# Kernel tuning notes

Measured on AMD Instinct MI355X. Metric: run time of the kernel, lower is better.

## Reference

```python
import jax, jax.numpy as jnp
import numpy as np

DIM = 1024
E = 8
K = 2
EPS = 1e-5

def _ln(x, g, b):
    mu = jnp.mean(x, axis=-1, keepdims=True)
    var = jnp.mean(jnp.square(x - mu), axis=-1, keepdims=True)
    return (x - mu) * jax.lax.rsqrt(var + EPS) * g + b

def setup_inputs() -> dict:
    key = jax.random.key(0)
    ks = jax.random.split(key, 8)
    H = 2 * DIM
    s_in = 1.0 / np.sqrt(DIM)
    s_h = 1.0 / np.sqrt(H)
    return {
        "x": jax.random.normal(ks[0], (2, 2048, DIM), dtype=jnp.float32),
        "gate_w": jax.random.uniform(ks[1], (DIM, E), minval=-s_in, maxval=s_in, dtype=jnp.float32),
        "w1": jax.random.uniform(ks[2], (E, DIM, H), minval=-s_in, maxval=s_in, dtype=jnp.float32),
        "b1": jax.random.uniform(ks[3], (E, H), minval=-s_in, maxval=s_in, dtype=jnp.float32),
        "ln1_g": jnp.ones((E, H), dtype=jnp.float32),
        "ln1_b": jnp.zeros((E, H), dtype=jnp.float32),
        "w2": jax.random.uniform(ks[4], (E, H, DIM), minval=-s_h, maxval=s_h, dtype=jnp.float32),
        "b2": jax.random.uniform(ks[5], (E, DIM), minval=-s_h, maxval=s_h, dtype=jnp.float32),
        "ln_g": jnp.ones((DIM,), dtype=jnp.float32),
        "ln_b": jnp.zeros((DIM,), dtype=jnp.float32),
    }

def reference(x, gate_w, w1, b1, ln1_g, ln1_b, w2, b2, ln_g, ln_b):
    shape = x.shape
    xf = x.reshape(-1, shape[-1])                      # [T, D]
    gates = jax.nn.softmax(xf @ gate_w, axis=-1)       # [T, E]
    topw, topi = jax.lax.top_k(gates, K)               # [T, K]
    topw = topw / jnp.sum(topw, axis=-1, keepdims=True)
    # combine weights per expert: [T, E]
    combine = jnp.sum(topw[:, :, None] * jax.nn.one_hot(topi, E, dtype=xf.dtype), axis=1)
    # run all experts on all tokens (vectorized grouped GEMM), combine by gate mask
    h = jnp.einsum('td,edh->teh', xf, w1) + b1          # [T, E, 2D]
    h = _ln(h, ln1_g, ln1_b)
    h = jax.nn.gelu(h, approximate=False)
    y = jnp.einsum('teh,ehd->ted', h, w2) + b2          # [T, E, D]
    out = jnp.einsum('ted,te->td', y, combine)          # [T, D]
    out = _ln(out + xf, ln_g, ln_b)
    return out.reshape(shape)
```

## Files before the change

### kernel.cpp

```cpp
#include <hip/hip_runtime.h>
#include <hip/hip_bf16.h>

#define DIMX 1024
#define HID  2048
#define NE   8
#define NT   4096
#define NPAIR 8192
#define MAXSTRIP 72

typedef __attribute__((ext_vector_type(8))) __bf16 bf16x8;
typedef __attribute__((ext_vector_type(4))) float f32x4;

__device__ inline unsigned short f2bf(float f) {
  union { float f; unsigned u; } v; v.f = f;
  unsigned r = v.u + 0x7FFFu + ((v.u >> 16) & 1u);
  return (unsigned short)(r >> 16);
}
__device__ inline float bf2f(unsigned short h) {
  union { unsigned u; float f; } v; v.u = ((unsigned)h) << 16;
  return v.f;
}

__device__ __forceinline__ void gload_lds16(const unsigned short* g, unsigned short* l) {
  __builtin_amdgcn_global_load_lds(
      (const __attribute__((address_space(1))) unsigned int*)g,
      (__attribute__((address_space(3))) unsigned int*)l, 16, 0, 0);
}

#define O_CNT   0u
#define O_TOK   1024u
#define O_TK    132096u
#define O_PW    263168u
#define O_TI    394240u
#define O_TW    427008u
#define O_POFF  459776u
#define O_SE    459904u
#define O_SR0   460416u
#define O_XBF   524288u
#define O_W1T   16777216u
#define O_W2T   50331648u
#define O_H     83886080u
#define O_Y     121634816u

__global__ __launch_bounds__(256) void k_gate_cvt(const float* __restrict__ x,
                                                  const float* __restrict__ gw,
                                                  unsigned short* __restrict__ xbf,
                                                  int* __restrict__ ti,
                                                  float* __restrict__ tw) {
  int t = blockIdx.x * 4 + (threadIdx.x >> 6);
  int lane = threadIdx.x & 63;
  const float4* xr = (const float4*)(x + (size_t)t * DIMX);
  ushort4* xo = (ushort4*)(xbf + (size_t)t * DIMX);
  float p[NE];
#pragma unroll
  for (int e = 0; e < NE; e++) p[e] = 0.f;
#pragma unroll
  for (int j = 0; j < 4; j++) {
    int idx4 = j * 64 + lane;
    float4 v = xr[idx4];
    ushort4 o; o.x = f2bf(v.x); o.y = f2bf(v.y); o.z = f2bf(v.z); o.w = f2bf(v.w);
    xo[idx4] = o;
    const float4* gp = (const float4*)(gw + (size_t)(idx4 * 4) * NE);
    float4 gA = gp[0], gB = gp[1], gC = gp[2], gD = gp[3];
    float4 gE = gp[4], gF = gp[5], gG = gp[6], gH = gp[7];
    p[0] += v.x * gA.x + v.y * gC.x + v.z * gE.x + v.w * gG.x;
    p[1] += v.x * gA.y + v.y * gC.y + v.z * gE.y + v.w * gG.y;
    p[2] += v.x * gA.z + v.y * gC.z + v.z * gE.z + v.w * gG.z;
    p[3] += v.x * gA.w + v.y * gC.w + v.z * gE.w + v.w * gG.w;
    p[4] += v.x * gB.x + v.y * gD.x + v.z * gF.x + v.w * gH.x;
    p[5] += v.x * gB.y + v.y * gD.y + v.z * gF.y + v.w * gH.y;
    p[6] += v.x * gB.z + v.y * gD.z + v.z * gF.z + v.w * gH.z;
    p[7] += v.x * gB.w + v.y * gD.w + v.z * gF.w + v.w * gH.w;
  }
#pragma unroll
  for (int e = 0; e < NE; e++)
#pragma unroll
    for (int off = 32; off > 0; off >>= 1) p[e] += __shfl_xor(p[e], off);
  if (lane == 0) {
    int ia = 0; float va = p[0];
#pragma unroll
    for (int e = 1; e < NE; e++) if (p[e] > va) { va = p[e]; ia = e; }
    int ib = -1; float vb = -3.0e38f;
#pragma unroll
    for (int e = 0; e < NE; e++) { if (e == ia) continue; if (p[e] > vb) { vb = p[e]; ib = e; } }
    float w0 = 1.f / (1.f + expf(vb - va));
    ti[t * 2] = ia;     tw[t * 2] = w0;
    ti[t * 2 + 1] = ib; tw[t * 2 + 1] = 1.f - w0;
  }
}

__global__ __launch_bounds__(512) void k_build(const int* __restrict__ ti,
                                               const float* __restrict__ tw,
                                               int* __restrict__ cnt,
                                               int* __restrict__ poffs,
                                               int* __restrict__ s_e, int* __restrict__ s_r0,
                                               int* __restrict__ ptok, int* __restrict__ ptk,
                                               float* __restrict__ pw) {
  __shared__ int sti[NPAIR];
  __shared__ float stw[NPAIR];
  __shared__ int scnt[NE];
  for (int i = threadIdx.x; i < NPAIR; i += 512) { sti[i] = ti[i]; stw[i] = tw[i]; }
  __syncthreads();
  int wid = threadIdx.x >> 6;
  int lane = threadIdx.x & 63;
  int c = 0;
  for (int p = lane; p < NPAIR; p += 64) c += (sti[p] == wid) ? 1 : 0;
#pragma unroll
  for (int off = 32; off > 0; off >>= 1) c += __shfl_xor(c, off);
  if (lane == 0) scnt[wid] = c;
  __syncthreads();
  if (threadIdx.x == 0) {
    int s = 0, pacc = 0;
    for (int e = 0; e < NE; e++) {
      cnt[e] = scnt[e];
      poffs[e] = pacc;
      int ns = (scnt[e] + 127) >> 7;
      for (int k = 0; k < ns; k++) { s_e[s] = e; s_r0[s] = k * 128; s++; }
      pacc += ns * 128;
    }
    poffs[NE] = pacc;
    for (; s < MAXSTRIP; s++) { s_e[s] = -1; s_r0[s] = 0; }
  }
  int base = 0;
  for (int p0 = 0; p0 < NPAIR; p0 += 64) {
    int p = p0 + lane;
    bool m = (sti[p] == wid);
    unsigned long long mask = __ballot(m);
    if (m) {
      int pos = base + __popcll(mask & ((1ull << lane) - 1ull));
      ptok[wid * NT + pos] = p >> 1;
      ptk[wid * NT + pos] = p;
      pw[wid * NT + pos] = stw[p];
    }
    base += __popcll(mask);
  }
}

__global__ __launch_bounds__(256) void k_transpose_cvt(const float* __restrict__ in,
                                                       unsigned short* __restrict__ out,
                                                       int R, int C) {
  __shared__ float tile[64][73];
  int e = blockIdx.z;
  const float* ip = in + (size_t)e * R * C;
  unsigned short* op = out + (size_t)e * R * C;
  int c0 = blockIdx.x * 64, r0 = blockIdx.y * 64;
  int tx = threadIdx.x & 15, ty = threadIdx.x >> 4;
#pragma unroll
  for (int i = 0; i < 4; i++) {
    int row = ty + i * 16;
    float4 v = *(const float4*)(ip + (size_t)(r0 + row) * C + c0 + tx * 4);
    tile[row][tx * 4] = v.x; tile[row][tx * 4 + 1] = v.y;
    tile[row][tx * 4 + 2] = v.z; tile[row][tx * 4 + 3] = v.w;
  }
  __syncthreads();
  int rx = threadIdx.x & 15, cy = threadIdx.x >> 4;
  int r_off = rx * 4;
#pragma unroll
  for (int i = 0; i < 4; i++) {
    int cc = cy + i * 16;
    ushort4 h;
    h.x = f2bf(tile[r_off][cc]);     h.y = f2bf(tile[r_off + 1][cc]);
    h.z = f2bf(tile[r_off + 2][cc]); h.w = f2bf(tile[r_off + 3][cc]);
    *(ushort4*)(op + (size_t)(c0 + cc) * R + r0 + r_off) = h;
  }
}

#define BM 128
#define BN 128
#define BK 32

__global__ __launch_bounds__(256) void k_gemm1(
    const unsigned short* __restrict__ xbf,
    const unsigned short* __restrict__ w1t,
    const float* __restrict__ bias1,
    const int* __restrict__ cnt, const int* __restrict__ s_e,
    const int* __restrict__ s_r0, const int* __restrict__ poffs,
    const int* __restrict__ ptok,
    unsigned short* __restrict__ hpre)
{
  int s = blockIdx.y;
  int e = s_e[s];
  if (e < 0) return;
  int r0e = s_r0[s];
  int n_e = cnt[e];
  int pbase = poffs[e];
  int col0 = blockIdx.x * BN;

  __shared__ __align__(16) unsigned short As[2][BM][BK];
  __shared__ __align__(16) unsigned short Bs[2][BN][BK];

  int tid = threadIdx.x;
  int lane = tid & 63, wid = tid >> 6;
  int wr = wid >> 1, wc = wid & 1;
  int quad = lane >> 4, m16 = lane & 15;

  int rr = lane >> 2;
  int csrc = ((lane & 3) ^ ((lane >> 3) & 3)) * 8;
  int ga0 = r0e + wid * 32 + rr;      if (ga0 >= n_e) ga0 = n_e - 1;
  int ga1 = r0e + wid * 32 + 16 + rr; if (ga1 >= n_e) ga1 = n_e - 1;
  int t0 = ptok[e * NT + ga0];
  int t1 = ptok[e * NT + ga1];
  const unsigned short* a0p = xbf + (size_t)t0 * DIMX + csrc;
  const unsigned short* a1p = xbf + (size_t)t1 * DIMX + csrc;
  const unsigned short* bbase = w1t + (size_t)e * HID * DIMX;
  const unsigned short* b0p = bbase + (size_t)(col0 + wid * 32 + rr) * DIMX + csrc;
  const unsigned short* b1p = bbase + (size_t)(col0 + wid * 32 + 16 + rr) * DIMX + csrc;

  int ca = (quad ^ ((m16 >> 1) & 3)) * 8;

  f32x4 acc[4][4];
#pragma unroll
  for (int i = 0; i < 4; i++)
#pragma unroll
    for (int j = 0; j < 4; j++) acc[i][j] = (f32x4)(0.f);

#define STAGE1(b, kk) do { \
    gload_lds16(a0p + (kk), &As[b][wid * 32][0]); \
    gload_lds16(a1p + (kk), &As[b][wid * 32 + 16][0]); \
    gload_lds16(b0p + (kk), &Bs[b][wid * 32][0]); \
    gload_lds16(b1p + (kk), &Bs[b][wid * 32 + 16][0]); \
  } while (0)

  STAGE1(0, 0);
  __syncthreads();
  int cur = 0;
  for (int k0 = 0; k0 < DIMX; k0 += BK) {
    if (k0 + BK < DIMX) STAGE1(cur ^ 1, k0 + BK);
    bf16x8 af[4], bfr[4];
#pragma unroll
    for (int i = 0; i < 4; i++) af[i]  = *(const bf16x8*)&As[cur][wr * 64 + i * 16 + m16][ca];
#pragma unroll
    for (int j = 0; j < 4; j++) bfr[j] = *(const bf16x8*)&Bs[cur][wc * 64 + j * 16 + m16][ca];
#pragma unroll
    for (int i = 0; i < 4; i++)
#pragma unroll
      for (int j = 0; j < 4; j++)
        acc[i][j] = __builtin_amdgcn_mfma_f32_16x16x32_bf16(af[i], bfr[j], acc[i][j], 0, 0, 0);
    __syncthreads();
    cur ^= 1;
  }
#undef STAGE1

  float bj[4];
#pragma unroll
  for (int j = 0; j < 4; j++) bj[j] = bias1[e * HID + col0 + wc * 64 + j * 16 + m16];
#pragma unroll
  for (int i = 0; i < 4; i++) {
#pragma unroll
    for (int r = 0; r < 4; r++) {
      int g = r0e + wr * 64 + i * 16 + quad * 4 + r;
      if (g < n_e) {
        size_t rowbase = (size_t)(pbase + g) * HID;
#pragma unroll
        for (int j = 0; j < 4; j++) {
          int colg = col0 + wc * 64 + j * 16 + m16;
          hpre[rowbase + colg] = f2bf(acc[i][j][r] + bj[j]);
        }
      }
    }
  }
}

__global__ __launch_bounds__(256) void k_ln_gelu(unsigned short* __restrict__ h,
                                                 const float* __restrict__ g1,
                                                 const float* __restrict__ bb1,
                                                 const int* __restrict__ s_e) {
  int row = blockIdx.x * 4 + (threadIdx.x >> 6);
  int e = s_e[row >> 7];
  if (e < 0) return;
  int lane = threadIdx.x & 63;
  unsigned short* p = h + (size_t)row * HID;
  int4* p4 = (int4*)p;
  int4 raw[4];
#pragma unroll
  for (int sg = 0; sg < 4; sg++) raw[sg] = p4[sg * 64 + lane];
  float v[32];
#pragma unroll
  for (int sg = 0; sg < 4; sg++) {
    const unsigned short* u = (const unsigned short*)&raw[sg];
#pragma unroll
    for (int k = 0; k < 8; k++) v[sg * 8 + k] = bf2f(u[k]);
  }
  float s = 0.f;
#pragma unroll
  for (int i = 0; i < 32; i++) s += v[i];
#pragma unroll
  for (int off = 32; off > 0; off >>= 1) s += __shfl_xor(s, off);
  float mean = s * (1.f / HID);
  float sq = 0.f;
#pragma unroll
  for (int i = 0; i < 32; i++) { float d = v[i] - mean; sq += d * d; }
#pragma unroll
  for (int off = 32; off > 0; off >>= 1) sq += __shfl_xor(sq, off);
  float rstd = rsqrtf(sq * (1.f / HID) + 1e-5f);
  const float4* gg = (const float4*)(g1 + (size_t)e * HID);
  const float4* gb = (const float4*)(bb1 + (size_t)e * HID);
#pragma unroll
  for (int sg = 0; sg < 4; sg++) {
    float4 ga = gg[sg * 128 + lane * 2], gc = gg[sg * 128 + lane * 2 + 1];
    float4 ba = gb[sg * 128 + lane * 2], bc = gb[sg * 128 + lane * 2 + 1];
    float gn[8] = {ga.x, ga.y, ga.z, ga.w, gc.x, gc.y, gc.z, gc.w};
    float bn[8] = {ba.x, ba.y, ba.z, ba.w, bc.x, bc.y, bc.z, bc.w};
    unsigned short o[8];
#pragma unroll
    for (int k = 0; k < 8; k++) {
      float xn = (v[sg * 8 + k] - mean) * rstd * gn[k] + bn[k];
      float ge = 0.5f * xn * (1.f + erff(xn * 0.7071067811865476f));
      o[k] = f2bf(ge);
    }
    p4[sg * 64 + lane] = *(const int4*)o;
  }
}

__global__ __launch_bounds__(256) void k_gemm2(
    const unsigned short* __restrict__ hb,
    const unsigned short* __restrict__ w2t,
    const float* __restrict__ bias2,
    const int* __restrict__ cnt, const int* __restrict__ s_e,
    const int* __restrict__ s_r0, const int* __restrict__ poffs,
    const int* __restrict__ ptk, const float* __restrict__ pw,
    float* __restrict__ ybuf)
{
  int s = blockIdx.y;
  int e = s_e[s];
  if (e < 0) return;
  int r0e = s_r0[s];
  int n_e = cnt[e];
  int pbase = poffs[e];
  int col0 = blockIdx.x * BN;

  __shared__ __align__(16) unsigned short As[2][BM][BK];
  __shared__ __align__(16) unsigned short Bs[2][BN][BK];

  int tid = threadIdx.x;
  int lane = tid & 63, wid = tid >> 6;
  int wr = wid >> 1, wc = wid & 1;
  int quad = lane >> 4, m16 = lane & 15;

  int rr = lane >> 2;
  int csrc = ((lane & 3) ^ ((lane >> 3) & 3)) * 8;
  int ga0 = r0e + wid * 32 + rr;      if (ga0 >= n_e) ga0 = n_e - 1;
  int ga1 = r0e + wid * 32 + 16 + rr; if (ga1 >= n_e) ga1 = n_e - 1;
  const unsigned short* a0p = hb + (size_t)(pbase + ga0) * HID + csrc;
  const unsigned short* a1p = hb + (size_t)(pbase + ga1) * HID + csrc;
  const unsigned short* bbase = w2t + (size_t)e * DIMX * HID;
  const unsigned short* b0p = bbase + (size_t)(col0 + wid * 32 + rr) * HID + csrc;
  const unsigned short* b1p = bbase + (size_t)(col0 + wid * 32 + 16 + rr) * HID + csrc;

  int ca = (quad ^ ((m16 >> 1) & 3)) * 8;

  f32x4 acc[4][4];
#pragma unroll
  for (int i = 0; i < 4; i++)
#pragma unroll
    for (int j = 0; j < 4; j++) acc[i][j] = (f32x4)(0.f);

#define STAGE2(b, kk) do { \
    gload_lds16(a0p + (kk), &As[b][wid * 32][0]); \
    gload_lds16(a1p + (kk), &As[b][wid * 32 + 16][0]); \
    gload_lds16(b0p + (kk), &Bs[b][wid * 32][0]); \
    gload_lds16(b1p + (kk), &Bs[b][wid * 32 + 16][0]); \
  } while (0)

  STAGE2(0, 0);
  __syncthreads();
  int cur = 0;
  for (int k0 = 0; k0 < HID; k0 += BK) {
    if (k0 + BK < HID) STAGE2(cur ^ 1, k0 + BK);
    bf16x8 af[4], bfr[4];
#pragma unroll
    for (int i = 0; i < 4; i++) af[i]  = *(const bf16x8*)&As[cur][wr * 64 + i * 16 + m16][ca];
#pragma unroll
    for (int j = 0; j < 4; j++) bfr[j] = *(const bf16x8*)&Bs[cur][wc * 64 + j * 16 + m16][ca];
#pragma unroll
    for (int i = 0; i < 4; i++)
#pragma unroll
      for (int j = 0; j < 4; j++)
        acc[i][j] = __builtin_amdgcn_mfma_f32_16x16x32_bf16(af[i], bfr[j], acc[i][j], 0, 0, 0);
    __syncthreads();
    cur ^= 1;
  }
#undef STAGE2

  float bj[4];
#pragma unroll
  for (int j = 0; j < 4; j++) bj[j] = bias2[e * DIMX + col0 + wc * 64 + j * 16 + m16];
#pragma unroll
  for (int i = 0; i < 4; i++) {
#pragma unroll
    for (int r = 0; r < 4; r++) {
      int g = r0e + wr * 64 + i * 16 + quad * 4 + r;
      if (g < n_e) {
        int pi = e * NT + g;
        float w = pw[pi];
        size_t obase = (size_t)ptk[pi] * DIMX;
#pragma unroll
        for (int j = 0; j < 4; j++) {
          int colg = col0 + wc * 64 + j * 16 + m16;
          ybuf[obase + colg] = (acc[i][j][r] + bj[j]) * w;
        }
      }
    }
  }
}

__global__ __launch_bounds__(256) void k_final(const float* __restrict__ yb,
                                               const float* __restrict__ x,
                                               const float* __restrict__ lg,
                                               const float* __restrict__ lb,
                                               float* __restrict__ out) {
  int t = blockIdx.x * 4 + (threadIdx.x >> 6);
  int lane = threadIdx.x & 63;
  const float4* y0 = (const float4*)(yb + (size_t)t * 2 * DIMX);
  const float4* y1 = y0 + DIMX / 4;
  const float4* x4 = (const float4*)(x + (size_t)t * DIMX);
  float4 v[4];
  float s = 0.f;
#pragma unroll
  for (int sg = 0; sg < 4; sg++) {
    int idx = sg * 64 + lane;
    float4 a = y0[idx], b = y1[idx], c = x4[idx];
    v[sg].x = a.x + b.x + c.x; v[sg].y = a.y + b.y + c.y;
    v[sg].z = a.z + b.z + c.z; v[sg].w = a.w + b.w + c.w;
    s += v[sg].x + v[sg].y + v[sg].z + v[sg].w;
  }
#pragma unroll
  for (int off = 32; off > 0; off >>= 1) s += __shfl_xor(s, off);
  float mean = s * (1.f / DIMX);
  float sq = 0.f;
#pragma unroll
  for (int sg = 0; sg < 4; sg++) {
    float dx = v[sg].x - mean, dy = v[sg].y - mean, dz = v[sg].z - mean, dw = v[sg].w - mean;
    sq += dx * dx + dy * dy + dz * dz + dw * dw;
  }
#pragma unroll
  for (int off = 32; off > 0; off >>= 1) sq += __shfl_xor(sq, off);
  float rstd = rsqrtf(sq * (1.f / DIMX) + 1e-5f);
  float4* o4 = (float4*)(out + (size_t)t * DIMX);
#pragma unroll
  for (int sg = 0; sg < 4; sg++) {
    int idx = sg * 64 + lane;
    float4 g = ((const float4*)lg)[idx], bb = ((const float4*)lb)[idx];
    float4 o;
    o.x = (v[sg].x - mean) * rstd * g.x + bb.x;
    o.y = (v[sg].y - mean) * rstd * g.y + bb.y;
    o.z = (v[sg].z - mean) * rstd * g.z + bb.z;
    o.w = (v[sg].w - mean) * rstd * g.w + bb.w;
    o4[idx] = o;
  }
}

extern "C" void kernel_launch(void* const* d_in, const int* in_sizes, int n_in,
                              void* d_out, int out_size, void* d_ws, size_t ws_size,
                              hipStream_t stream) {
  const float* x     = (const float*)d_in[0];
  const float* gw    = (const float*)d_in[1];
  const float* w1    = (const float*)d_in[2];
  const float* b1    = (const float*)d_in[3];
  const float* ln1g  = (const float*)d_in[4];
  const float* ln1b  = (const float*)d_in[5];
  const float* w2    = (const float*)d_in[6];
  const float* b2    = (const float*)d_in[7];
  const float* lng   = (const float*)d_in[8];
  const float* lnb   = (const float*)d_in[9];
  float* out = (float*)d_out;

  char* ws = (char*)d_ws;
  int* cnt   = (int*)(ws + O_CNT);
  int* ptok  = (int*)(ws + O_TOK);
  int* ptk   = (int*)(ws + O_TK);
  float* pw  = (float*)(ws + O_PW);
  int* ti    = (int*)(ws + O_TI);
  float* tw  = (float*)(ws + O_TW);
  int* poffs = (int*)(ws + O_POFF);
  int* s_e   = (int*)(ws + O_SE);
  int* s_r0  = (int*)(ws + O_SR0);
  unsigned short* xbf  = (unsigned short*)(ws + O_XBF);
  unsigned short* w1t  = (unsigned short*)(ws + O_W1T);
  unsigned short* w2t  = (unsigned short*)(ws + O_W2T);
  unsigned short* hpre = (unsigned short*)(ws + O_H);
  float* ybuf = (float*)(ws + O_Y);

  hipLaunchKernelGGL(k_gate_cvt, dim3(NT / 4), dim3(256), 0, stream, x, gw, xbf, ti, tw);
  hipLaunchKernelGGL(k_build, dim3(1), dim3(512), 0, stream, ti, tw, cnt, poffs, s_e, s_r0,
                     ptok, ptk, pw);
  hipLaunchKernelGGL(k_transpose_cvt, dim3(HID / 64, DIMX / 64, NE), dim3(256), 0, stream,
                     w1, w1t, DIMX, HID);
  hipLaunchKernelGGL(k_transpose_cvt, dim3(DIMX / 64, HID / 64, NE), dim3(256), 0, stream,
                     w2, w2t, HID, DIMX);
  hipLaunchKernelGGL(k_gemm1, dim3(HID / BN, MAXSTRIP), dim3(256), 0, stream,
                     xbf, w1t, b1, cnt, s_e, s_r0, poffs, ptok, hpre);
  hipLaunchKernelGGL(k_ln_gelu, dim3(MAXSTRIP * BM / 4), dim3(256), 0, stream,
                     hpre, ln1g, ln1b, s_e);
  hipLaunchKernelGGL(k_gemm2, dim3(DIMX / BN, MAXSTRIP), dim3(256), 0, stream,
                     hpre, w2t, b2, cnt, s_e, s_r0, poffs, ptk, pw, ybuf);
  hipLaunchKernelGGL(k_final, dim3(NT / 4), dim3(256), 0, stream, ybuf, x, lng, lnb, out);
}
```

Baseline: 385.3 us.

## Split-K gemm2 into two halves and remap blocks across XCDs

The second expert GEMM is split along K into two halves launched as a third grid dimension. Each half writes its partial result to its own buffer, with the bias added only by the second half. The second buffer reuses the w1t workspace, which is dead once gemm1 has run. The final LayerNorm kernel now sums both partial buffers. Both GEMMs also remap linear block ids so that blocks for the same strip land on the same XCD for L2 locality. The aim is to double gemm2 parallelism so it fills more CUs; the cost is extra partial-sum traffic in the final kernel.

Result: no change. 385.9 us (+0.2%).

```diff
diff --git a/kernel.cpp b/kernel.cpp
--- a/kernel.cpp
+++ b/kernel.cpp
@@ -178,13 +178,17 @@
     const int* __restrict__ ptok,
     unsigned short* __restrict__ hpre)
 {
-  int s = blockIdx.y;
+  int lid = blockIdx.x + 16 * blockIdx.y;
+  int xcd = lid & 7;
+  int t4 = lid >> 3;
+  int colb = t4 & 15;
+  int s = xcd * 9 + (t4 >> 4);
   int e = s_e[s];
   if (e < 0) return;
   int r0e = s_r0[s];
   int n_e = cnt[e];
   int pbase = poffs[e];
-  int col0 = blockIdx.x * BN;
+  int col0 = colb * BN;
 
   __shared__ __align__(16) unsigned short As[2][BM][BK];
   __shared__ __align__(16) unsigned short Bs[2][BN][BK];
@@ -319,15 +323,22 @@
     const int* __restrict__ cnt, const int* __restrict__ s_e,
     const int* __restrict__ s_r0, const int* __restrict__ poffs,
     const int* __restrict__ ptk, const float* __restrict__ pw,
-    float* __restrict__ ybuf)
+    float* __restrict__ ybufA, float* __restrict__ ybufB)
 {
-  int s = blockIdx.y;
+  int lid = blockIdx.x + 8 * (blockIdx.y + 72 * blockIdx.z);
+  int xcd = lid & 7;
+  int t4 = lid >> 3;
+  int colb = t4 & 7;
+  int rem = t4 >> 3;
+  int ks = rem & 1;
+  int s = xcd * 9 + (rem >> 1);
   int e = s_e[s];
   if (e < 0) return;
   int r0e = s_r0[s];
   int n_e = cnt[e];
   int pbase = poffs[e];
-  int col0 = blockIdx.x * BN;
+  int col0 = colb * BN;
+  int kbase = ks << 10;
 
   __shared__ __align__(16) unsigned short As[2][BM][BK];
   __shared__ __align__(16) unsigned short Bs[2][BN][BK];
@@ -341,11 +352,11 @@
   int csrc = ((lane & 3) ^ ((lane >> 3) & 3)) * 8;
   int ga0 = r0e + wid * 32 + rr;      if (ga0 >= n_e) ga0 = n_e - 1;
   int ga1 = r0e + wid * 32 + 16 + rr; if (ga1 >= n_e) ga1 = n_e - 1;
-  const unsigned short* a0p = hb + (size_t)(pbase + ga0) * HID + csrc;
-  const unsigned short* a1p = hb + (size_t)(pbase + ga1) * HID + csrc;
+  const unsigned short* a0p = hb + (size_t)(pbase + ga0) * HID + kbase + csrc;
+  const unsigned short* a1p = hb + (size_t)(pbase + ga1) * HID + kbase + csrc;
   const unsigned short* bbase = w2t + (size_t)e * DIMX * HID;
-  const unsigned short* b0p = bbase + (size_t)(col0 + wid * 32 + rr) * HID + csrc;
-  const unsigned short* b1p = bbase + (size_t)(col0 + wid * 32 + 16 + rr) * HID + csrc;
+  const unsigned short* b0p = bbase + (size_t)(col0 + wid * 32 + rr) * HID + kbase + csrc;
+  const unsigned short* b1p = bbase + (size_t)(col0 + wid * 32 + 16 + rr) * HID + kbase + csrc;
 
   int ca = (quad ^ ((m16 >> 1) & 3)) * 8;
 
@@ -365,8 +376,8 @@
   STAGE2(0, 0);
   __syncthreads();
   int cur = 0;
-  for (int k0 = 0; k0 < HID; k0 += BK) {
-    if (k0 + BK < HID) STAGE2(cur ^ 1, k0 + BK);
+  for (int k0 = 0; k0 < HID / 2; k0 += BK) {
+    if (k0 + BK < HID / 2) STAGE2(cur ^ 1, k0 + BK);
     bf16x8 af[4], bfr[4];
 #pragma unroll
     for (int i = 0; i < 4; i++) af[i]  = *(const bf16x8*)&As[cur][wr * 64 + i * 16 + m16][ca];
@@ -382,9 +393,11 @@
   }
 #undef STAGE2
 
+  float* yb = ks ? ybufB : ybufA;
   float bj[4];
 #pragma unroll
-  for (int j = 0; j < 4; j++) bj[j] = bias2[e * DIMX + col0 + wc * 64 + j * 16 + m16];
+  for (int j = 0; j < 4; j++)
+    bj[j] = ks ? bias2[e * DIMX + col0 + wc * 64 + j * 16 + m16] : 0.f;
 #pragma unroll
   for (int i = 0; i < 4; i++) {
 #pragma unroll
@@ -397,31 +410,36 @@
 #pragma unroll
         for (int j = 0; j < 4; j++) {
           int colg = col0 + wc * 64 + j * 16 + m16;
-          ybuf[obase + colg] = (acc[i][j][r] + bj[j]) * w;
+          yb[obase + colg] = (acc[i][j][r] + bj[j]) * w;
         }
       }
     }
   }
 }
 
-__global__ __launch_bounds__(256) void k_final(const float* __restrict__ yb,
+__global__ __launch_bounds__(256) void k_final(const float* __restrict__ ybA,
+                                               const float* __restrict__ ybB,
                                                const float* __restrict__ x,
                                                const float* __restrict__ lg,
                                                const float* __restrict__ lb,
                                                float* __restrict__ out) {
   int t = blockIdx.x * 4 + (threadIdx.x >> 6);
   int lane = threadIdx.x & 63;
-  const float4* y0 = (const float4*)(yb + (size_t)t * 2 * DIMX);
-  const float4* y1 = y0 + DIMX / 4;
+  const float4* yA0 = (const float4*)(ybA + (size_t)t * 2 * DIMX);
+  const float4* yA1 = yA0 + DIMX / 4;
+  const float4* yB0 = (const float4*)(ybB + (size_t)t * 2 * DIMX);
+  const float4* yB1 = yB0 + DIMX / 4;
   const float4* x4 = (const float4*)(x + (size_t)t * DIMX);
   float4 v[4];
   float s = 0.f;
 #pragma unroll
   for (int sg = 0; sg < 4; sg++) {
     int idx = sg * 64 + lane;
-    float4 a = y0[idx], b = y1[idx], c = x4[idx];
-    v[sg].x = a.x + b.x + c.x; v[sg].y = a.y + b.y + c.y;
-    v[sg].z = a.z + b.z + c.z; v[sg].w = a.w + b.w + c.w;
+    float4 a = yA0[idx], b = yA1[idx], a2 = yB0[idx], b2 = yB1[idx], c = x4[idx];
+    v[sg].x = a.x + b.x + a2.x + b2.x + c.x;
+    v[sg].y = a.y + b.y + a2.y + b2.y + c.y;
+    v[sg].z = a.z + b.z + a2.z + b2.z + c.z;
+    v[sg].w = a.w + b.w + a2.w + b2.w + c.w;
     s += v[sg].x + v[sg].y + v[sg].z + v[sg].w;
   }
 #pragma unroll
@@ -479,7 +497,8 @@
   unsigned short* w1t  = (unsigned short*)(ws + O_W1T);
   unsigned short* w2t  = (unsigned short*)(ws + O_W2T);
   unsigned short* hpre = (unsigned short*)(ws + O_H);
-  float* ybuf = (float*)(ws + O_Y);
+  float* ybufA = (float*)(ws + O_Y);
+  float* ybufB = (float*)(ws + O_W1T);
 
   hipLaunchKernelGGL(k_gate_cvt, dim3(NT / 4), dim3(256), 0, stream, x, gw, xbf, ti, tw);
   hipLaunchKernelGGL(k_build, dim3(1), dim3(512), 0, stream, ti, tw, cnt, poffs, s_e, s_r0,
@@ -492,7 +511,7 @@
                      xbf, w1t, b1, cnt, s_e, s_r0, poffs, ptok, hpre);
   hipLaunchKernelGGL(k_ln_gelu, dim3(MAXSTRIP * BM / 4), dim3(256), 0, stream,
                      hpre, ln1g, ln1b, s_e);
-  hipLaunchKernelGGL(k_gemm2, dim3(DIMX / BN, MAXSTRIP), dim3(256), 0, stream,
-                     hpre, w2t, b2, cnt, s_e, s_r0, poffs, ptk, pw, ybuf);
-  hipLaunchKernelGGL(k_final, dim3(NT / 4), dim3(256), 0, stream, ybuf, x, lng, lnb, out);
-}
+  hipLaunchKernelGGL(k_gemm2, dim3(DIMX / BN, MAXSTRIP, 2), dim3(256), 0, stream,
+                     hpre, w2t, b2, cnt, s_e, s_r0, poffs, ptk, pw, ybufA, ybufB);
+  hipLaunchKernelGGL(k_final, dim3(NT / 4), dim3(256), 0, stream, ybufA, ybufB, x, lng, lnb, out);
+}
```
